# Kernel tuning notes

Hardware: AMD Instinct MI355X
Metric: run time of the kernel (lower is better)

The kernel has to match this reference:

```python
import jax, jax.numpy as jnp
import numpy as np

T, H, E, I, K, G, KG = 16384, 1024, 64, 768, 8, 8, 4


def setup_inputs() -> dict:
    key = jax.random.key(0)
    ks = jax.random.split(key, 6)
    return {
        "hidden_states": jax.random.normal(ks[0], (T, H), jnp.float32),
        "gate_weight": jax.random.normal(ks[1], (E, H), jnp.float32) * 0.02,
        "correction_bias": jax.random.normal(ks[2], (E,), jnp.float32) * 0.01,
        "w_gate": jax.random.normal(ks[3], (E, I, H), jnp.float32) * 0.02,
        "w_up": jax.random.normal(ks[4], (E, I, H), jnp.float32) * 0.02,
        "w_down": jax.random.normal(ks[5], (E, H, I), jnp.float32) * 0.02,
    }


def _grouped_topk(hidden, gate_w, bias, top_k=K, n_group=G, topk_group=KG, renormalize=True):
    # gate runs in fp32 (MoEGate.dtype = float32)
    logits = hidden.astype(jnp.float32) @ gate_w.T  # [T, E]
    scores = jax.nn.sigmoid(logits)  # noaux_tc uses sigmoid scores
    s_choice = scores + bias[None, :].astype(jnp.float32)
    t, e = scores.shape
    # group score = sum of top-2 biased scores within each group
    grouped = s_choice.reshape(t, n_group, e // n_group)
    top2, _ = jax.lax.top_k(grouped, 2)
    group_scores = top2.sum(-1)  # [T, G]
    _, gidx = jax.lax.top_k(group_scores, topk_group)  # [T, KG]
    gmask = jnp.zeros((t, n_group), jnp.float32).at[jnp.arange(t)[:, None], gidx].set(1.0)
    emask = jnp.repeat(gmask, e // n_group, axis=1)  # [T, E]
    masked = jnp.where(emask > 0, s_choice, -jnp.inf)
    _, topk_idx = jax.lax.top_k(masked, top_k)  # [T, K]
    # weights use the unbiased sigmoid scores
    topk_w = jnp.take_along_axis(scores, topk_idx, axis=1)
    if renormalize:
        topk_w = topk_w / (topk_w.sum(-1, keepdims=True) + 1e-20)
    # routed_scaling_factor = 1.0
    return topk_idx, topk_w


def reference(hidden_states, gate_weight, correction_bias, w_gate, w_up, w_down):
    t = hidden_states.shape[0]
    topk_idx, topk_w = _grouped_topk(hidden_states, gate_weight, correction_bias)
    # dense combine weights [T, E]: zero except at selected experts
    combine = jnp.zeros((t, E), hidden_states.dtype).at[
        jnp.arange(t)[:, None], topk_idx
    ].add(topk_w.astype(hidden_states.dtype))

    def step(acc, xs):
        wg, wu, wd, c = xs  # wg/wu: [I,H], wd: [H,I], c: [T]
        h = jax.nn.silu(hidden_states @ wg.T) * (hidden_states @ wu.T)  # [T, I]
        return acc + c[:, None] * (h @ wd.T), None

    acc0 = jnp.zeros_like(hidden_states)
    out, _ = jax.lax.scan(step, acc0, (w_gate, w_up, w_down, combine.T))
    return out
```

## Files before the change

kernel.cpp:

```cpp
#include <hip/hip_runtime.h>
#include <hip/hip_bf16.h>
#include <math.h>

#define T_TOK 16384
#define H_DIM 1024
#define E_NUM 64
#define I_DIM 768
#define TOPK  8
#define NGRP  8
#define KGRP  4
#define S_ASN (T_TOK*TOPK)
#define BM 128
#define BK 64
#define MAXBLK (S_ASN/BM + E_NUM)

typedef __attribute__((ext_vector_type(4))) float f4v;
typedef __attribute__((ext_vector_type(8))) short s8v;
typedef __attribute__((ext_vector_type(4))) unsigned short u4sv;

#define GLDS16(g, l) __builtin_amdgcn_global_load_lds( \
    (const __attribute__((address_space(1))) void*)(g), \
    (__attribute__((address_space(3))) void*)(l), 16, 0, 0)

static __device__ __forceinline__ short f2bf(float f){
  union { float f; unsigned u; } a; a.f = f;
  unsigned u = a.u;
  unsigned r = (u + 0x7fffu + ((u >> 16) & 1u)) >> 16;
  return (short)r;
}
static __device__ __forceinline__ float bf2f(unsigned short h){
  union { unsigned u; float f; } a; a.u = ((unsigned)h) << 16; return a.f;
}
static __device__ __forceinline__ s8v cvt8(f4v a, f4v b){
  s8v r;
  r[0]=f2bf(a[0]); r[1]=f2bf(a[1]); r[2]=f2bf(a[2]); r[3]=f2bf(a[3]);
  r[4]=f2bf(b[0]); r[5]=f2bf(b[1]); r[6]=f2bf(b[2]); r[7]=f2bf(b[3]);
  return r;
}

__launch_bounds__(256)
__global__ void cast_kernel(const float* __restrict__ src,
                            short* __restrict__ dst, long n8)
{
  long i = (long)blockIdx.x*blockDim.x + threadIdx.x;
  long stride = (long)gridDim.x*blockDim.x;
  for (; i < n8; i += stride){
    f4v a = __builtin_nontemporal_load((const f4v*)(src + i*8));
    f4v b = __builtin_nontemporal_load((const f4v*)(src + i*8 + 4));
    __builtin_nontemporal_store(cvt8(a, b), (s8v*)(dst + i*8));
  }
}

__launch_bounds__(256)
__global__ void gate_kernel(const float* __restrict__ hidden,
                            const float* __restrict__ gate_w,
                            double* __restrict__ logits,
                            short*  __restrict__ hb)
{
  __shared__ float sX[64][33];
  __shared__ float sW[64][33];
  const int tid  = threadIdx.x;
  const int t0   = blockIdx.x * 64;
  const int srow = tid >> 2;
  const int scol = (tid & 3) * 8;
  const int tx = tid & 15, ty = tid >> 4;
  double acc[4][4];
  #pragma unroll
  for (int i=0;i<4;i++)
    #pragma unroll
    for (int j=0;j<4;j++) acc[i][j]=0.0;

  for (int k0=0;k0<H_DIM;k0+=32){
    f4v a0 = *(const f4v*)&hidden[(size_t)(t0+srow)*H_DIM + k0 + scol];
    f4v a1 = *(const f4v*)&hidden[(size_t)(t0+srow)*H_DIM + k0 + scol + 4];
    f4v b0 = *(const f4v*)&gate_w[(size_t)srow*H_DIM + k0 + scol];
    f4v b1 = *(const f4v*)&gate_w[(size_t)srow*H_DIM + k0 + scol + 4];
    if (hb)
      *(s8v*)&hb[(size_t)(t0+srow)*H_DIM + k0 + scol] = cvt8(a0, a1);
    __syncthreads();
    #pragma unroll
    for (int j=0;j<4;j++){
      sX[srow][scol+j]   = a0[j];  sX[srow][scol+4+j] = a1[j];
      sW[srow][scol+j]   = b0[j];  sW[srow][scol+4+j] = b1[j];
    }
    __syncthreads();
    #pragma unroll
    for (int kk=0;kk<32;kk++){
      float xv[4], wv[4];
      #pragma unroll
      for (int i=0;i<4;i++){ xv[i]=sX[ty*4+i][kk]; wv[i]=sW[tx*4+i][kk]; }
      #pragma unroll
      for (int i=0;i<4;i++)
        #pragma unroll
        for (int j=0;j<4;j++)
          acc[i][j] += (double)xv[i] * (double)wv[j];
    }
  }
  #pragma unroll
  for (int i=0;i<4;i++)
    #pragma unroll
    for (int j=0;j<4;j++)
      logits[(size_t)(t0+ty*4+i)*E_NUM + tx*4+j] = acc[i][j];
}

__global__ void route_kernel(const double* __restrict__ logits,
                             const float*  __restrict__ bias,
                             int*   __restrict__ topk_idx,
                             float* __restrict__ topk_w,
                             int*   __restrict__ counts)
{
  const int t = blockIdx.x * blockDim.x + threadIdx.x;
  if (t >= T_TOK) return;
  const double* lg = logits + (size_t)t * E_NUM;
  double sc[E_NUM], sch[E_NUM];
  for (int e2=0;e2<E_NUM;e2++){
    double s = 1.0 / (1.0 + exp(-lg[e2]));
    sc[e2]  = s;
    sch[e2] = s + (double)bias[e2];
  }
  double gs[NGRP];
  for (int g=0;g<NGRP;g++){
    double m1=-1e300, m2=-1e300;
    for (int j=0;j<8;j++){
      double v = sch[g*8+j];
      if (v > m1){ m2 = m1; m1 = v; } else if (v > m2){ m2 = v; }
    }
    gs[g] = m1 + m2;
  }
  unsigned gsel = 0;
  for (int r=0;r<KGRP;r++){
    int best = 0; double bv = -1.0e308;
    for (int g=0;g<NGRP;g++)
      if (!((gsel>>g)&1u) && gs[g] > bv){ bv = gs[g]; best = g; }
    gsel |= 1u << best;
  }
  unsigned long long used = 0ULL;
  double wsum = 0.0;
  int sel[TOPK]; double w[TOPK];
  for (int r=0;r<TOPK;r++){
    int best = 0; double bv = -1.0e308;
    for (int e2=0;e2<E_NUM;e2++){
      if ((used>>e2)&1ULL) continue;
      if (!((gsel>>(e2>>3))&1u)) continue;
      if (sch[e2] > bv){ bv = sch[e2]; best = e2; }
    }
    used |= 1ULL << best;
    sel[r] = best;
    w[r]   = sc[best];
    wsum  += w[r];
  }
  double inv = 1.0 / (wsum + 1e-20);
  for (int r=0;r<TOPK;r++){
    topk_idx[(size_t)t*TOPK + r] = sel[r];
    topk_w  [(size_t)t*TOPK + r] = (float)(w[r]*inv);
    atomicAdd(&counts[sel[r]], 1);
  }
}

__global__ void scan_kernel(const int* __restrict__ counts,
                            int* __restrict__ offsets,
                            int* __restrict__ blk_start)
{
  if (threadIdx.x == 0 && blockIdx.x == 0){
    int off = 0, blk = 0;
    for (int e=0;e<E_NUM;e++){
      offsets[e] = off; blk_start[e] = blk;
      off += counts[e];
      blk += (counts[e] + BM - 1) / BM;
    }
    offsets[E_NUM] = off; blk_start[E_NUM] = blk;
  }
}

__global__ void scatter_kernel(const int* __restrict__ topk_idx,
                               const float* __restrict__ topk_w,
                               const int* __restrict__ offsets,
                               int* __restrict__ cursor,
                               int* __restrict__ token_list,
                               float* __restrict__ weight_list,
                               int* __restrict__ pos_list)
{
  const int t = blockIdx.x*blockDim.x + threadIdx.x;
  if (t >= T_TOK) return;
  for (int r=0;r<TOPK;r++){
    int   e2 = topk_idx[(size_t)t*TOPK + r];
    float wv = topk_w [(size_t)t*TOPK + r];
    int p = atomicAdd(&cursor[e2], 1);
    token_list [offsets[e2] + p] = t;
    weight_list[offsets[e2] + p] = wv;
    pos_list[(size_t)t*TOPK + r] = offsets[e2] + p;
  }
}


__launch_bounds__(512, 4)
__global__ void ffn1_fast(const short* __restrict__ hid_bf,
                          const short* __restrict__ wg_bf,
                          const short* __restrict__ wu_bf,
                          const int*   __restrict__ token_list,
                          const float* __restrict__ weight_list,
                          const int*   __restrict__ offsets,
                          const int*   __restrict__ blk_start,
                          short*       __restrict__ h_all)
{
  __shared__ short lsX[128*64];
  __shared__ short lsG[128*64];
  __shared__ short lsU[128*64];
  __shared__ float lsWt[128];

  const int bx = blockIdx.x;
  if (bx >= blk_start[E_NUM]) return;
  int e = 0;
  while (blk_start[e+1] <= bx) ++e;
  const int rb   = bx - blk_start[e];
  const int cb   = blockIdx.y;
  const int base = offsets[e];
  const int n_e  = offsets[e+1] - base;
  const int row0 = rb * BM;

  const int tid = threadIdx.x;
  const int lane = tid & 63, wid = tid >> 6;
  const int wm = wid >> 2, wn = wid & 3;
  const int l15 = lane & 15, l4 = lane >> 4;

  if (tid < BM) lsWt[tid] = ((row0+tid) < n_e) ? weight_list[base+row0+tid] : 0.f;

  const short* srcA[2];
  #pragma unroll
  for (int i=0;i<2;i++){
    int s_lin = i*512 + tid;
    int row = s_lin >> 3, sl = s_lin & 7;
    int asn = base + row0 + row; if (asn >= S_ASN) asn = S_ASN-1;
    int tok = token_list[asn];
    srcA[i] = hid_bf + (size_t)tok*H_DIM + ((sl ^ (row&7))<<3);
  }
  const short* srcG[2]; const short* srcU[2];
  #pragma unroll
  for (int i=0;i<2;i++){
    int s_lin = i*512 + tid;
    int row = s_lin >> 3, sl = s_lin & 7;
    size_t wrow = ((size_t)e*I_DIM + cb*128 + row)*H_DIM + ((sl ^ (row&7))<<3);
    srcG[i] = wg_bf + wrow;
    srcU[i] = wu_bf + wrow;
  }
  short* dstA0 = lsX + wid*512;
  short* dstG0 = lsG + wid*512;
  short* dstU0 = lsU + wid*512;

  f4v accg[4][2], accu[4][2];
  #pragma unroll
  for (int m=0;m<4;m++)
    #pragma unroll
    for (int n=0;n<2;n++){
      accg[m][n]=(f4v){0.f,0.f,0.f,0.f};
      accu[m][n]=(f4v){0.f,0.f,0.f,0.f};
    }

  for (int k0=0; k0<H_DIM; k0+=BK){
    __syncthreads();
    #pragma unroll
    for (int i=0;i<2;i++) GLDS16(srcA[i]+k0, dstA0 + i*4096);
    #pragma unroll
    for (int i=0;i<2;i++) GLDS16(srcG[i]+k0, dstG0 + i*4096);
    #pragma unroll
    for (int i=0;i<2;i++) GLDS16(srcU[i]+k0, dstU0 + i*4096);
    __syncthreads();
    #pragma unroll
    for (int kk=0;kk<2;kk++){
      s8v af[4], bg[2], bu[2];
      #pragma unroll
      for (int m=0;m<4;m++){
        int r = wm*64 + m*16 + l15;
        int s = (kk*4 + l4) ^ (r & 7);
        af[m] = *(const s8v*)&lsX[r*64 + (s<<3)];
      }
      #pragma unroll
      for (int n=0;n<2;n++){
        int r = wn*32 + n*16 + l15;
        int s = (kk*4 + l4) ^ (r & 7);
        bg[n] = *(const s8v*)&lsG[r*64 + (s<<3)];
        bu[n] = *(const s8v*)&lsU[r*64 + (s<<3)];
      }
      #pragma unroll
      for (int m=0;m<4;m++)
        #pragma unroll
        for (int n=0;n<2;n++){
          accg[m][n] = __builtin_amdgcn_mfma_f32_16x16x32_bf16(af[m], bg[n], accg[m][n], 0,0,0);
          accu[m][n] = __builtin_amdgcn_mfma_f32_16x16x32_bf16(af[m], bu[n], accu[m][n], 0,0,0);
        }
    }
  }
  #pragma unroll
  for (int m=0;m<4;m++){
    #pragma unroll
    for (int i=0;i<4;i++){
      int r = wm*64 + m*16 + l4*4 + i;
      if (row0 + r < n_e){
        float wgt = lsWt[r];
        size_t hb = (size_t)(base+row0+r)*I_DIM + (size_t)cb*128;
        #pragma unroll
        for (int n=0;n<2;n++){
          int c = wn*32 + n*16 + l15;
          float g = accg[m][n][i], u = accu[m][n][i];
          float s = g / (1.f + __expf(-g));
          h_all[hb + c] = f2bf(s * u * wgt);
        }
      }
    }
  }
}

__launch_bounds__(256, 3)
__global__ void ffn2y_fast(const short* __restrict__ h_all,
                           const short* __restrict__ wd_bf,
                           const int*   __restrict__ offsets,
                           const int*   __restrict__ blk_start,
                           short*       __restrict__ y,
                           int          cb0)
{
  __shared__ short lsA[128*64];
  __shared__ short lsB[128*64];

  const int bx = blockIdx.x;
  if (bx >= blk_start[E_NUM]) return;
  int e = 0;
  while (blk_start[e+1] <= bx) ++e;
  const int rb   = bx - blk_start[e];
  const int cby  = blockIdx.y;
  const int cbg  = cb0*4 + cby;
  const int base = offsets[e];
  const int n_e  = offsets[e+1] - base;
  const int row0 = rb * BM;

  const int tid = threadIdx.x;
  const int lane = tid & 63, wid = tid >> 6;
  const int wm = wid >> 1, wn = wid & 1;
  const int l15 = lane & 15, l4 = lane >> 4;

  const short* srcA[4]; const short* srcB[4];
  #pragma unroll
  for (int i=0;i<4;i++){
    int s_lin = i*256 + tid;
    int row = s_lin >> 3, sl = s_lin & 7;
    int arow = base + row0 + row; if (arow >= S_ASN) arow = S_ASN-1;
    srcA[i] = h_all + (size_t)arow*I_DIM + ((sl ^ (row&7))<<3);
    srcB[i] = wd_bf + ((size_t)e*H_DIM + cbg*128 + row)*I_DIM + ((sl ^ (row&7))<<3);
  }
  short* dstA0 = lsA + wid*512;
  short* dstB0 = lsB + wid*512;

  f4v acc[4][4];
  #pragma unroll
  for (int m=0;m<4;m++)
    #pragma unroll
    for (int n=0;n<4;n++) acc[m][n]=(f4v){0.f,0.f,0.f,0.f};

  for (int k0=0; k0<I_DIM; k0+=BK){
    __syncthreads();
    #pragma unroll
    for (int i=0;i<4;i++) GLDS16(srcA[i]+k0, dstA0 + i*2048);
    #pragma unroll
    for (int i=0;i<4;i++) GLDS16(srcB[i]+k0, dstB0 + i*2048);
    __syncthreads();
    #pragma unroll
    for (int kk=0;kk<2;kk++){
      s8v af[4], bf[4];
      #pragma unroll
      for (int m=0;m<4;m++){
        int r = wm*64 + m*16 + l15;
        int s = (kk*4 + l4) ^ (r & 7);
        af[m] = *(const s8v*)&lsA[r*64 + (s<<3)];
      }
      #pragma unroll
      for (int n=0;n<4;n++){
        int r = wn*64 + n*16 + l15;
        int s = (kk*4 + l4) ^ (r & 7);
        bf[n] = *(const s8v*)&lsB[r*64 + (s<<3)];
      }
      #pragma unroll
      for (int m=0;m<4;m++)
        #pragma unroll
        for (int n=0;n<4;n++)
          acc[m][n] = __builtin_amdgcn_mfma_f32_16x16x32_bf16(af[m], bf[n], acc[m][n], 0,0,0);
    }
  }
  #pragma unroll
  for (int m=0;m<4;m++){
    #pragma unroll
    for (int i=0;i<4;i++){
      int r = wm*64 + m*16 + l4*4 + i;
      if (row0 + r < n_e){
        size_t yb = (size_t)(base+row0+r)*512 + (size_t)cby*128;
        #pragma unroll
        for (int n=0;n<4;n++){
          int c = wn*64 + n*16 + l15;
          y[yb + c] = f2bf(acc[m][n][i]);
        }
      }
    }
  }
}

__launch_bounds__(256)
__global__ void combine_kernel(const short* __restrict__ y,
                               const int*   __restrict__ pos,
                               float*       __restrict__ out,
                               int cb0)
{
  const int tid = threadIdx.x;
  const int t = blockIdx.x*2 + (tid >> 7);
  const int c = (tid & 127) * 4;
  const int* pp = pos + (size_t)t*TOPK;
  float s0=0.f, s1=0.f, s2=0.f, s3=0.f;
  #pragma unroll
  for (int r=0;r<TOPK;r++){
    int row = pp[r];
    u4sv v = *(const u4sv*)&y[(size_t)row*512 + c];
    s0 += bf2f(v[0]); s1 += bf2f(v[1]); s2 += bf2f(v[2]); s3 += bf2f(v[3]);
  }
  f4v o = {s0,s1,s2,s3};
  *(f4v*)&out[(size_t)t*H_DIM + (size_t)cb0*512 + c] = o;
}

__launch_bounds__(512, 2)
__global__ void ffn1_kernel(const float* __restrict__ hidden,
                            const float* __restrict__ w_gate,
                            const float* __restrict__ w_up,
                            const int*   __restrict__ token_list,
                            const float* __restrict__ weight_list,
                            const int*   __restrict__ offsets,
                            const int*   __restrict__ blk_start,
                            short*       __restrict__ h_all)
{
  __shared__ short lsX[BM*64];
  __shared__ short lsG[BM*64];
  __shared__ short lsU[BM*64];
  __shared__ float lsWt[BM];

  const int bx = blockIdx.x;
  if (bx >= blk_start[E_NUM]) return;
  int e = 0;
  while (blk_start[e+1] <= bx) ++e;
  const int rb   = bx - blk_start[e];
  const int cb   = blockIdx.y;
  const int base = offsets[e];
  const int n_e  = offsets[e+1] - base;
  const int row0 = rb * BM;

  const int tid   = threadIdx.x;
  const int srow  = tid >> 2;
  const int scol  = (tid & 3) << 4;
  const int slot0 = (tid & 3) << 1;
  const int wsl0  = srow*64 + (((slot0  ) ^ (srow & 7)) << 3);
  const int wsl1  = srow*64 + (((slot0+1) ^ (srow & 7)) << 3);

  const bool tvalid = (row0 + srow) < n_e;
  int tok = 0;
  if (tvalid) tok = token_list[base + row0 + srow];
  const float* xsrc = hidden + (size_t)tok * H_DIM + scol;
  const size_t woff = (size_t)e * I_DIM * H_DIM + (size_t)(cb*128 + srow) * H_DIM + scol;
  const float* gsrc = w_gate + woff;
  const float* usrc = w_up   + woff;

  const int lane = tid & 63, wid = tid >> 6;
  const int wm = wid >> 2, wn = wid & 3;
  const int l15 = lane & 15, l4 = lane >> 4;

  f4v accg[4][2], accu[4][2];
  #pragma unroll
  for (int m=0;m<4;m++)
    #pragma unroll
    for (int n=0;n<2;n++){
      accg[m][n]=(f4v){0.f,0.f,0.f,0.f};
      accu[m][n]=(f4v){0.f,0.f,0.f,0.f};
    }

  for (int k0=0; k0<H_DIM; k0+=BK){
    f4v x0,x1,x2,x3;
    if (tvalid){
      x0 = *(const f4v*)(xsrc+k0);   x1 = *(const f4v*)(xsrc+k0+4);
      x2 = *(const f4v*)(xsrc+k0+8); x3 = *(const f4v*)(xsrc+k0+12);
    } else {
      x0=x1=x2=x3=(f4v){0.f,0.f,0.f,0.f};
    }
    f4v g0 = *(const f4v*)(gsrc+k0),   g1 = *(const f4v*)(gsrc+k0+4);
    f4v g2 = *(const f4v*)(gsrc+k0+8), g3 = *(const f4v*)(gsrc+k0+12);
    f4v u0 = *(const f4v*)(usrc+k0),   u1 = *(const f4v*)(usrc+k0+4);
    f4v u2 = *(const f4v*)(usrc+k0+8), u3 = *(const f4v*)(usrc+k0+12);
    __syncthreads();
    *(s8v*)&lsX[wsl0] = cvt8(x0,x1);  *(s8v*)&lsX[wsl1] = cvt8(x2,x3);
    *(s8v*)&lsG[wsl0] = cvt8(g0,g1);  *(s8v*)&lsG[wsl1] = cvt8(g2,g3);
    *(s8v*)&lsU[wsl0] = cvt8(u0,u1);  *(s8v*)&lsU[wsl1] = cvt8(u2,u3);
    __syncthreads();
    #pragma unroll
    for (int kk=0;kk<2;kk++){
      s8v af[4], bg[2], bu[2];
      #pragma unroll
      for (int m=0;m<4;m++){
        int r = wm*64 + m*16 + l15;
        int s = (kk*4 + l4) ^ (r & 7);
        af[m] = *(const s8v*)&lsX[r*64 + (s<<3)];
      }
      #pragma unroll
      for (int n=0;n<2;n++){
        int r = wn*32 + n*16 + l15;
        int s = (kk*4 + l4) ^ (r & 7);
        bg[n] = *(const s8v*)&lsG[r*64 + (s<<3)];
        bu[n] = *(const s8v*)&lsU[r*64 + (s<<3)];
      }
      #pragma unroll
      for (int m=0;m<4;m++)
        #pragma unroll
        for (int n=0;n<2;n++){
          accg[m][n] = __builtin_amdgcn_mfma_f32_16x16x32_bf16(af[m], bg[n], accg[m][n], 0,0,0);
          accu[m][n] = __builtin_amdgcn_mfma_f32_16x16x32_bf16(af[m], bu[n], accu[m][n], 0,0,0);
        }
    }
  }
  if (tid < BM) lsWt[tid] = ((row0+tid) < n_e) ? weight_list[base+row0+tid] : 0.f;
  __syncthreads();
  #pragma unroll
  for (int m=0;m<4;m++){
    #pragma unroll
    for (int i=0;i<4;i++){
      int r = wm*64 + m*16 + l4*4 + i;
      if (row0 + r < n_e){
        float wgt = lsWt[r];
        size_t hb = (size_t)(base+row0+r)*I_DIM + (size_t)cb*128;
        #pragma unroll
        for (int n=0;n<2;n++){
          int c = wn*32 + n*16 + l15;
          float g = accg[m][n][i], u = accu[m][n][i];
          float s = g / (1.f + __expf(-g));
          h_all[hb + c] = f2bf(s * u * wgt);
        }
      }
    }
  }
}

__launch_bounds__(512, 2)
__global__ void ffn2_kernel(const short* __restrict__ h_all,
                            const float* __restrict__ w_down,
                            const int*   __restrict__ token_list,
                            const int*   __restrict__ offsets,
                            const int*   __restrict__ blk_start,
                            float*       __restrict__ out)
{
  __shared__ short lsA[BM*64];
  __shared__ short lsB[BM*64];
  __shared__ int   lsT[BM];

  const int bx = blockIdx.x;
  if (bx >= blk_start[E_NUM]) return;
  int e = 0;
  while (blk_start[e+1] <= bx) ++e;
  const int rb   = bx - blk_start[e];
  const int cb   = blockIdx.y;
  const int base = offsets[e];
  const int n_e  = offsets[e+1] - base;
  const int row0 = rb * BM;

  const int tid   = threadIdx.x;
  const int srow  = tid >> 2;
  const int slot0 = (tid & 3) << 1;
  const int wsl0  = srow*64 + (((slot0  ) ^ (srow & 7)) << 3);
  const int wsl1  = srow*64 + (((slot0+1) ^ (srow & 7)) << 3);

  int arow = base + row0 + srow;
  if (arow >= S_ASN) arow = S_ASN - 1;
  const short* asrc = h_all + (size_t)arow*I_DIM + ((tid&3)<<4);
  const float* bsrc = w_down + (size_t)e*H_DIM*I_DIM
                    + (size_t)(cb*128 + srow)*I_DIM + ((tid&3)<<4);

  const int lane = tid & 63, wid = tid >> 6;
  const int wm = wid >> 2, wn = wid & 3;
  const int l15 = lane & 15, l4 = lane >> 4;

  f4v acc[4][2];
  #pragma unroll
  for (int m=0;m<4;m++)
    #pragma unroll
    for (int n=0;n<2;n++) acc[m][n]=(f4v){0.f,0.f,0.f,0.f};

  for (int k0=0; k0<I_DIM; k0+=BK){
    s8v alo = *(const s8v*)(asrc + k0);
    s8v ahi = *(const s8v*)(asrc + k0 + 8);
    f4v b0 = *(const f4v*)(bsrc+k0),   b1 = *(const f4v*)(bsrc+k0+4);
    f4v b2 = *(const f4v*)(bsrc+k0+8), b3 = *(const f4v*)(bsrc+k0+12);
    __syncthreads();
    *(s8v*)&lsA[wsl0] = alo;          *(s8v*)&lsA[wsl1] = ahi;
    *(s8v*)&lsB[wsl0] = cvt8(b0,b1);  *(s8v*)&lsB[wsl1] = cvt8(b2,b3);
    __syncthreads();
    #pragma unroll
    for (int kk=0;kk<2;kk++){
      s8v af[4], bf[2];
      #pragma unroll
      for (int m=0;m<4;m++){
        int r = wm*64 + m*16 + l15;
        int s = (kk*4 + l4) ^ (r & 7);
        af[m] = *(const s8v*)&lsA[r*64 + (s<<3)];
      }
      #pragma unroll
      for (int n=0;n<2;n++){
        int r = wn*32 + n*16 + l15;
        int s = (kk*4 + l4) ^ (r & 7);
        bf[n] = *(const s8v*)&lsB[r*64 + (s<<3)];
      }
      #pragma unroll
      for (int m=0;m<4;m++)
        #pragma unroll
        for (int n=0;n<2;n++)
          acc[m][n] = __builtin_amdgcn_mfma_f32_16x16x32_bf16(af[m], bf[n], acc[m][n], 0,0,0);
    }
  }
  if (tid < BM) lsT[tid] = ((row0+tid) < n_e) ? token_list[base+row0+tid] : -1;
  __syncthreads();
  #pragma unroll
  for (int m=0;m<4;m++){
    #pragma unroll
    for (int i=0;i<4;i++){
      int r = wm*64 + m*16 + l4*4 + i;
      int tk = lsT[r];
      if (tk >= 0){
        #pragma unroll
        for (int n=0;n<2;n++){
          int c = cb*128 + wn*32 + n*16 + l15;
          atomicAdd(&out[(size_t)tk*H_DIM + c], acc[m][n][i]);
        }
      }
    }
  }
}

extern "C" void kernel_launch(void* const* d_in, const int* in_sizes, int n_in,
                              void* d_out, int out_size, void* d_ws, size_t ws_size,
                              hipStream_t stream)
{
  const float* hidden = (const float*)d_in[0];
  const float* gate_w = (const float*)d_in[1];
  const float* bias   = (const float*)d_in[2];
  const float* w_gate = (const float*)d_in[3];
  const float* w_up   = (const float*)d_in[4];
  const float* w_down = (const float*)d_in[5];
  float* out = (float*)d_out;

  char* ws = (char*)d_ws;
  size_t off = 0;
  #define WALLOC(bytes) (ws + off); off += (((size_t)(bytes)) + 255) & ~(size_t)255
  double* logits    = (double*)WALLOC((size_t)T_TOK*E_NUM*8);
  int*    topk_idx  = (int*)   WALLOC((size_t)T_TOK*TOPK*4);
  float*  topk_w    = (float*) WALLOC((size_t)T_TOK*TOPK*4);
  int*    counts    = (int*)   WALLOC(256);
  int*    cursor    = (int*)   WALLOC(256);
  int*    offsets   = (int*)   WALLOC(512);
  int*    blk_st    = (int*)   WALLOC(512);
  int*    token_l   = (int*)   WALLOC((size_t)S_ASN*4);
  float*  weight_l  = (float*) WALLOC((size_t)S_ASN*4);
  int*    pos_l     = (int*)   WALLOC((size_t)S_ASN*4);
  short*  h_all     = (short*) WALLOC((size_t)S_ASN*I_DIM*2);
  const size_t base_need = off;
  short*  hid_bf    = (short*) WALLOC((size_t)T_TOK*H_DIM*2);
  short*  wg_bf     = (short*) WALLOC((size_t)E_NUM*I_DIM*H_DIM*2);
  short*  wu_bf     = (short*) WALLOC((size_t)E_NUM*I_DIM*H_DIM*2);
  short*  wd_bf     = (short*) WALLOC((size_t)E_NUM*H_DIM*I_DIM*2);
  const size_t fast_need = off;
  #undef WALLOC
  short* y_all = hid_bf;

  const bool fast = (ws_size >= fast_need);
  if (ws_size < base_need) return;

  hipMemsetAsync(counts, 0, 512, stream);

  gate_kernel   <<<T_TOK/64,  256, 0, stream>>>(hidden, gate_w, logits,
                                                fast ? hid_bf : (short*)0);
  route_kernel  <<<T_TOK/256, 256, 0, stream>>>(logits, bias, topk_idx, topk_w, counts);
  scan_kernel   <<<1, 64, 0, stream>>>(counts, offsets, blk_st);
  scatter_kernel<<<T_TOK/256, 256, 0, stream>>>(topk_idx, topk_w, offsets, cursor,
                                                token_l, weight_l, pos_l);
  if (fast){
    long n8w = (long)E_NUM*I_DIM*H_DIM/8;
    cast_kernel<<<3072, 256, 0, stream>>>(w_gate, wg_bf, n8w);
    cast_kernel<<<3072, 256, 0, stream>>>(w_up,   wu_bf, n8w);
    cast_kernel<<<3072, 256, 0, stream>>>(w_down, wd_bf, n8w);
    dim3 g1(MAXBLK, I_DIM/128);
    ffn1_fast<<<g1, 512, 0, stream>>>(hid_bf, wg_bf, wu_bf, token_l, weight_l,
                                      offsets, blk_st, h_all);
    dim3 g2(MAXBLK, 4);
    for (int half = 0; half < 2; ++half){
      ffn2y_fast<<<g2, 256, 0, stream>>>(h_all, wd_bf, offsets, blk_st,
                                         y_all, half);
      combine_kernel<<<T_TOK/2, 256, 0, stream>>>(y_all, pos_l, out, half);
    }
  } else {
    hipMemsetAsync(out, 0, (size_t)T_TOK*H_DIM*4, stream);
    dim3 g1(MAXBLK, I_DIM/128);
    ffn1_kernel<<<g1, 512, 0, stream>>>(hidden, w_gate, w_up, token_l, weight_l,
                                        offsets, blk_st, h_all);
    dim3 g2(MAXBLK, H_DIM/128);
    ffn2_kernel<<<g2, 512, 0, stream>>>(h_all, w_down, token_l, offsets, blk_st, out);
  }
}
```

Baseline: 1.697 ms.

## Swap grid axes for weight-tile reuse and run FFN2 in one full-width pass

The FFN1 and FFN2 grids are transposed so column blocks become the fast-varying index. Consecutive workgroups then share the same row block of activations and are more likely to reuse it in cache. The h_all output is written with nontemporal stores. When the workspace is large enough, a full-width y buffer (S_ASN x H) lets FFN2 run as a single launch instead of two halves, at the cost of more workspace memory and a larger intermediate write and read.

```diff
diff --git a/kernel.cpp b/kernel.cpp
--- a/kernel.cpp
+++ b/kernel.cpp
@@ -208,12 +208,12 @@
   __shared__ short lsU[128*64];
   __shared__ float lsWt[128];
 
-  const int bx = blockIdx.x;
+  const int bx = blockIdx.y;
   if (bx >= blk_start[E_NUM]) return;
   int e = 0;
   while (blk_start[e+1] <= bx) ++e;
   const int rb   = bx - blk_start[e];
-  const int cb   = blockIdx.y;
+  const int cb   = blockIdx.x;
   const int base = offsets[e];
   const int n_e  = offsets[e+1] - base;
   const int row0 = rb * BM;
@@ -303,7 +303,7 @@
           int c = wn*32 + n*16 + l15;
           float g = accg[m][n][i], u = accu[m][n][i];
           float s = g / (1.f + __expf(-g));
-          h_all[hb + c] = f2bf(s * u * wgt);
+          __builtin_nontemporal_store((short)f2bf(s * u * wgt), &h_all[hb + c]);
         }
       }
     }
@@ -316,17 +316,18 @@
                            const int*   __restrict__ offsets,
                            const int*   __restrict__ blk_start,
                            short*       __restrict__ y,
-                           int          cb0)
+                           int          cb0,
+                           int          ystride)
 {
   __shared__ short lsA[128*64];
   __shared__ short lsB[128*64];
 
-  const int bx = blockIdx.x;
+  const int bx = blockIdx.y;
   if (bx >= blk_start[E_NUM]) return;
   int e = 0;
   while (blk_start[e+1] <= bx) ++e;
   const int rb   = bx - blk_start[e];
-  const int cby  = blockIdx.y;
+  const int cby  = blockIdx.x;
   const int cbg  = cb0*4 + cby;
   const int base = offsets[e];
   const int n_e  = offsets[e+1] - base;
@@ -390,7 +391,7 @@
     for (int i=0;i<4;i++){
       int r = wm*64 + m*16 + l4*4 + i;
       if (row0 + r < n_e){
-        size_t yb = (size_t)(base+row0+r)*512 + (size_t)cby*128;
+        size_t yb = (size_t)(base+row0+r)*ystride + (size_t)cby*128;
         #pragma unroll
         for (int n=0;n<4;n++){
           int c = wn*64 + n*16 + l15;
@@ -405,7 +406,7 @@
 __global__ void combine_kernel(const short* __restrict__ y,
                                const int*   __restrict__ pos,
                                float*       __restrict__ out,
-                               int cb0)
+                               int cb0, int ystride, int ybase)
 {
   const int tid = threadIdx.x;
   const int t = blockIdx.x*2 + (tid >> 7);
@@ -415,7 +416,7 @@
   #pragma unroll
   for (int r=0;r<TOPK;r++){
     int row = pp[r];
-    u4sv v = *(const u4sv*)&y[(size_t)row*512 + c];
+    u4sv v = *(const u4sv*)&y[(size_t)row*ystride + ybase + c];
     s0 += bf2f(v[0]); s1 += bf2f(v[1]); s2 += bf2f(v[2]); s3 += bf2f(v[3]);
   }
   f4v o = {s0,s1,s2,s3};
@@ -665,10 +666,13 @@
   short*  wu_bf     = (short*) WALLOC((size_t)E_NUM*I_DIM*H_DIM*2);
   short*  wd_bf     = (short*) WALLOC((size_t)E_NUM*H_DIM*I_DIM*2);
   const size_t fast_need = off;
+  short*  y2        = (short*) WALLOC((size_t)S_ASN*H_DIM*2);
+  const size_t fast2_need = off;
   #undef WALLOC
   short* y_all = hid_bf;
 
-  const bool fast = (ws_size >= fast_need);
+  const bool fast  = (ws_size >= fast_need);
+  const bool fast2 = (ws_size >= fast2_need);
   if (ws_size < base_need) return;
 
   hipMemsetAsync(counts, 0, 512, stream);
@@ -684,14 +688,23 @@
     cast_kernel<<<3072, 256, 0, stream>>>(w_gate, wg_bf, n8w);
     cast_kernel<<<3072, 256, 0, stream>>>(w_up,   wu_bf, n8w);
     cast_kernel<<<3072, 256, 0, stream>>>(w_down, wd_bf, n8w);
-    dim3 g1(MAXBLK, I_DIM/128);
+    dim3 g1(I_DIM/128, MAXBLK);
     ffn1_fast<<<g1, 512, 0, stream>>>(hid_bf, wg_bf, wu_bf, token_l, weight_l,
                                       offsets, blk_st, h_all);
-    dim3 g2(MAXBLK, 4);
-    for (int half = 0; half < 2; ++half){
+    if (fast2){
+      dim3 g2(8, MAXBLK);
       ffn2y_fast<<<g2, 256, 0, stream>>>(h_all, wd_bf, offsets, blk_st,
-                                         y_all, half);
-      combine_kernel<<<T_TOK/2, 256, 0, stream>>>(y_all, pos_l, out, half);
+                                         y2, 0, H_DIM);
+      combine_kernel<<<T_TOK/2, 256, 0, stream>>>(y2, pos_l, out, 0, H_DIM, 0);
+      combine_kernel<<<T_TOK/2, 256, 0, stream>>>(y2, pos_l, out, 1, H_DIM, 512);
+    } else {
+      dim3 g2(4, MAXBLK);
+      for (int half = 0; half < 2; ++half){
+        ffn2y_fast<<<g2, 256, 0, stream>>>(h_all, wd_bf, offsets, blk_st,
+                                           y_all, half, 512);
+        combine_kernel<<<T_TOK/2, 256, 0, stream>>>(y_all, pos_l, out,
+                                                    half, 512, 0);
+      }
     }
   } else {
     hipMemsetAsync(out, 0, (size_t)T_TOK*H_DIM*4, stream);
```

Result: faster. 1.588 ms (-6.4%).
